# Optimization experiments

Measured on AMD Instinct MI355X. Metric: run time of the kernel, lower is better.

The kernel has to match this reference:

```python
import jax, jax.numpy as jnp
import numpy as np

N = 8192            # number of ROIs
FEAT = 255          # num_classes(151) + embed_dim(100) + pos_dim(4)
HID = 64
PRE_NMS = 6000      # eval-mode pre_nms_topn
POST_NMS = 300      # eval-mode post_nms_topn
NMS_THRESH = 0.7


def setup_inputs() -> dict:
    key = jax.random.key(0)
    ks = jax.random.split(key, 12)
    # rois: [N,5] = (im_ind, x1, y1, x2, y2), valid boxes in a 1024x1024 image
    x1 = jax.random.uniform(ks[0], (N,)) * 900.0
    y1 = jax.random.uniform(ks[1], (N,)) * 900.0
    w = jax.random.uniform(ks[2], (N,)) * 120.0 + 4.0
    h = jax.random.uniform(ks[3], (N,)) * 120.0 + 4.0
    rois = jnp.stack([jnp.zeros((N,)), x1, y1, x1 + w, y1 + h], axis=1).astype(jnp.float32)
    roi_feat = jax.random.normal(ks[4], (N, FEAT), dtype=jnp.float32)
    s = 0.05
    return {
        "rois": rois,
        "roi_feat": roi_feat,
        "W_sub1": jax.random.normal(ks[5], (FEAT, HID), jnp.float32) * s,
        "b_sub1": jnp.zeros((HID,), jnp.float32),
        "W_sub2": jax.random.normal(ks[6], (HID, HID), jnp.float32) * s,
        "b_sub2": jnp.zeros((HID,), jnp.float32),
        "W_obj1": jax.random.normal(ks[7], (FEAT, HID), jnp.float32) * s,
        "b_obj1": jnp.zeros((HID,), jnp.float32),
        "W_obj2": jax.random.normal(ks[8], (HID, HID), jnp.float32) * s,
        "b_obj2": jnp.zeros((HID,), jnp.float32),
    }


def _iou_matrix(boxes):
    # boxes: [K,4] (x1,y1,x2,y2) -> [K,K] IoU
    x1, y1, x2, y2 = boxes[:, 0], boxes[:, 1], boxes[:, 2], boxes[:, 3]
    area = (x2 - x1) * (y2 - y1)
    ix1 = jnp.maximum(x1[:, None], x1[None, :])
    iy1 = jnp.maximum(y1[:, None], y1[None, :])
    ix2 = jnp.minimum(x2[:, None], x2[None, :])
    iy2 = jnp.minimum(y2[:, None], y2[None, :])
    inter = jnp.maximum(ix2 - ix1, 0.0) * jnp.maximum(iy2 - iy1, 0.0)
    return inter / (area[:, None] + area[None, :] - inter + 1e-8)


def reference(rois, roi_feat, W_sub1, b_sub1, W_sub2, b_sub2,
              W_obj1, b_obj1, W_obj2, b_obj2):
    # Original detaches roi_feat before the bilinear head.
    f = jax.lax.stop_gradient(roi_feat)
    x_sub = jnp.maximum(f @ W_sub1 + b_sub1, 0.0) @ W_sub2 + b_sub2  # [N,64]
    x_obj = jnp.maximum(f @ W_obj1 + b_obj1, 0.0) @ W_obj2 + b_obj2  # [N,64]
    scores = jax.nn.sigmoid(x_sub @ x_obj.T)                          # [N,N]

    n = scores.shape[0]
    # exclude self-pairs (sub == obj)
    diag = jnp.arange(n)
    flat = scores.at[diag, diag].set(-1.0).reshape(-1)

    # pre-NMS top-k over all N*N pairs (sorted descending)
    top_s, top_i = jax.lax.top_k(flat, PRE_NMS)
    sub = top_i // n
    obj = top_i % n

    boxes = jax.lax.stop_gradient(rois[:, 1:5])
    bs, bo = boxes[sub], boxes[obj]
    # union box of each (sub,obj) pair for relation NMS
    union = jnp.concatenate([jnp.minimum(bs[:, :2], bo[:, :2]),
                             jnp.maximum(bs[:, 2:], bo[:, 2:])], axis=1)  # [PRE,4]
    iou = _iou_matrix(union)                                              # [PRE,PRE]
    # non-greedy (matrix) NMS: suppress i if any higher-ranked j overlaps > thresh
    higher = jnp.triu(jnp.ones((PRE_NMS, PRE_NMS), bool), k=1)  # [j,i] true when j < i
    suppressed = jnp.any((iou > NMS_THRESH) & higher, axis=0)
    kept_scores = jnp.where(suppressed, -1.0, top_s)

    post_s, post_k = jax.lax.top_k(kept_scores, POST_NMS)
    rel_inds = jnp.stack([sub[post_k], obj[post_k]], axis=1)  # [POST,2]
    return rel_inds, post_s
```

## Files before the change

kernel.cpp:

```cpp
#include <hip/hip_runtime.h>
#include <math.h>

#define NB    8192
#define FEAT  255
#define HID   64
#define TOPK  6000
#define POSTK 300
#define BINS  8192
#define BSHIFT 19
#define CAP   131072
#define CAPLIM 49152
#define SLACK 1
#define TSEL  1000
#define JSLICES 128
#define LCAP  2048
#define NMS_ICH 64

typedef __attribute__((ext_vector_type(8))) short bf16x8;
typedef __attribute__((ext_vector_type(4))) float f32x4;

__device__ __forceinline__ unsigned binOf(float x) {
    unsigned u = __float_as_uint(x);
    u = (u & 0x80000000u) ? ~u : (u | 0x80000000u);
    return u >> BSHIFT;
}

__device__ __forceinline__ unsigned short f2bf(float f) {
    unsigned u = __float_as_uint(f);
    return (unsigned short)((u + 0x7fffu + ((u >> 16) & 1u)) >> 16);
}

__global__ __launch_bounds__(256) void mlp_kernel(
    const float* __restrict__ feat,
    const float* __restrict__ W1s, const float* __restrict__ b1s,
    const float* __restrict__ W2s, const float* __restrict__ b2s,
    const float* __restrict__ W1o, const float* __restrict__ b1o,
    const float* __restrict__ W2o, const float* __restrict__ b2o,
    double* __restrict__ Xs64, double* __restrict__ Xo64,
    unsigned short* __restrict__ Xsb, unsigned short* __restrict__ Xob)
{
    int tid = threadIdx.x;
    int t   = tid & 63;
    int w   = tid >> 6;
    int rbase = blockIdx.x * 4;

    __shared__ double pS[4][4][64];
    __shared__ double pO[4][4][64];
    __shared__ double hs[4][64];
    __shared__ double ho[4][64];

    const float* f0 = feat + (size_t)(rbase + 0) * FEAT;
    const float* f1 = feat + (size_t)(rbase + 1) * FEAT;
    const float* f2 = feat + (size_t)(rbase + 2) * FEAT;
    const float* f3 = feat + (size_t)(rbase + 3) * FEAT;

    int kbeg = w * 64;
    int kend = kbeg + 64; if (kend > FEAT) kend = FEAT;
    double as[4] = {0, 0, 0, 0}, ao[4] = {0, 0, 0, 0};
#pragma unroll 4
    for (int k = kbeg; k < kend; ++k) {
        double ws = (double)W1s[k * HID + t];
        double wo = (double)W1o[k * HID + t];
        double g0 = (double)f0[k], g1 = (double)f1[k];
        double g2 = (double)f2[k], g3 = (double)f3[k];
        as[0] += g0 * ws; as[1] += g1 * ws; as[2] += g2 * ws; as[3] += g3 * ws;
        ao[0] += g0 * wo; ao[1] += g1 * wo; ao[2] += g2 * wo; ao[3] += g3 * wo;
    }
#pragma unroll
    for (int i = 0; i < 4; ++i) { pS[w][i][t] = as[i]; pO[w][i][t] = ao[i]; }
    __syncthreads();

    {
        double v = (double)b1s[t] + ((pS[0][w][t] + pS[1][w][t]) + (pS[2][w][t] + pS[3][w][t]));
        double u = (double)b1o[t] + ((pO[0][w][t] + pO[1][w][t]) + (pO[2][w][t] + pO[3][w][t]));
        hs[w][t] = v > 0.0 ? v : 0.0;
        ho[w][t] = u > 0.0 ? u : 0.0;
    }
    __syncthreads();

    int k2beg = w * 16, k2end = k2beg + 16;
    double xs[4] = {0, 0, 0, 0}, xo[4] = {0, 0, 0, 0};
#pragma unroll 4
    for (int k = k2beg; k < k2end; ++k) {
        double ws = (double)W2s[k * HID + t];
        double wo = (double)W2o[k * HID + t];
#pragma unroll
        for (int i = 0; i < 4; ++i) {
            xs[i] += hs[i][k] * ws;
            xo[i] += ho[i][k] * wo;
        }
    }
#pragma unroll
    for (int i = 0; i < 4; ++i) { pS[w][i][t] = xs[i]; pO[w][i][t] = xo[i]; }
    __syncthreads();

    {
        double v = (double)b2s[t] + ((pS[0][w][t] + pS[1][w][t]) + (pS[2][w][t] + pS[3][w][t]));
        double u = (double)b2o[t] + ((pO[0][w][t] + pO[1][w][t]) + (pO[2][w][t] + pO[3][w][t]));
        size_t o = (size_t)(rbase + w) * HID + t;
        Xs64[o] = v;
        Xo64[o] = u;
        Xsb[o] = f2bf((float)v);
        Xob[o] = f2bf((float)u);
    }
}

__global__ __launch_bounds__(256) void mfma_hist(
    const unsigned short* __restrict__ Xsb, const unsigned short* __restrict__ Xob,
    unsigned* __restrict__ ghist)
{
    __shared__ unsigned hist[BINS];
    int tid = threadIdx.x;
    for (int i = tid; i < BINS; i += 256) hist[i] = 0u;
    __syncthreads();

    int lane = tid & 63;
    int wave = tid >> 6;
    int quad = lane >> 4;
    int l16  = lane & 15;
    int r0 = blockIdx.y * 128 + (wave >> 1) * 64;
    int c0 = blockIdx.x * 128 + (wave & 1) * 64;

    f32x4 acc[4][4];
    bf16x8 afr[2][4], bfr[2][4];
#pragma unroll
    for (int kc = 0; kc < 2; ++kc)
#pragma unroll
        for (int t = 0; t < 4; ++t) {
            afr[kc][t] = *(const bf16x8*)(Xsb + (size_t)(r0 + t * 16 + l16) * HID + kc * 32 + quad * 8);
            bfr[kc][t] = *(const bf16x8*)(Xob + (size_t)(c0 + t * 16 + l16) * HID + kc * 32 + quad * 8);
        }
#pragma unroll
    for (int ti = 0; ti < 4; ++ti)
#pragma unroll
        for (int tj = 0; tj < 4; ++tj) acc[ti][tj] = (f32x4){0, 0, 0, 0};
#pragma unroll
    for (int kc = 0; kc < 2; ++kc)
#pragma unroll
        for (int ti = 0; ti < 4; ++ti)
#pragma unroll
            for (int tj = 0; tj < 4; ++tj)
                acc[ti][tj] = __builtin_amdgcn_mfma_f32_16x16x32_bf16(
                    afr[kc][ti], bfr[kc][tj], acc[ti][tj], 0, 0, 0);

#pragma unroll
    for (int ti = 0; ti < 4; ++ti)
#pragma unroll
        for (int tj = 0; tj < 4; ++tj)
#pragma unroll
            for (int i = 0; i < 4; ++i) {
                int r = r0 + ti * 16 + quad * 4 + i;
                int c = c0 + tj * 16 + l16;
                float v = acc[ti][tj][i];
                if (v > 0.0f && r != c)
                    atomicAdd(&hist[binOf(v)], 1u);
            }

    __syncthreads();
    for (int i = tid; i < BINS; i += 256) {
        unsigned h = hist[i];
        if (h) atomicAdd(&ghist[i], h);
    }
}

__global__ __launch_bounds__(256) void find_threshold(
    const unsigned* __restrict__ ghist, unsigned* __restrict__ ctrl)
{
    __shared__ unsigned csum[256];
    int tid  = threadIdx.x;
    int base = tid * (BINS / 256);
    unsigned s = 0;
    for (int i = 0; i < BINS / 256; ++i) s += ghist[base + i];
    csum[tid] = s;
    __syncthreads();
    if (tid == 0) {
        unsigned run = 0;
        for (int c = 255; c >= 0; --c) { run += csum[c]; csum[c] = run; }
    }
    __syncthreads();

    unsigned above = (tid == 255) ? 0u : csum[tid + 1];
    unsigned prev = above;
    for (int b = base + BINS / 256 - 1; b >= base; --b) {
        unsigned cur = prev + ghist[b];
        if (cur >= TSEL && prev < TSEL) {
            unsigned bstar = (unsigned)b;
            unsigned bt = bstar >= SLACK ? bstar - SLACK : 0;
            unsigned cnt = cur;
            for (unsigned bb = bstar; bb-- > bt;) cnt += ghist[bb];
            while (8u * cnt > CAPLIM && bt < bstar) { cnt -= ghist[bt]; bt++; }
            ctrl[1] = bt;
            unsigned key = bt << BSHIFT;
            unsigned fbits;
            if (key == 0u) fbits = 0xff800000u;
            else fbits = (key & 0x80000000u) ? (key ^ 0x80000000u) : ~key;
            ctrl[2] = fbits;
            break;
        }
        prev = cur;
    }
}

__global__ __launch_bounds__(256) void mfma_filter(
    const unsigned short* __restrict__ Xsb, const unsigned short* __restrict__ Xob,
    unsigned* __restrict__ ctrl, unsigned* __restrict__ cidx)
{
    __shared__ unsigned lcnt;
    __shared__ unsigned gbase;
    __shared__ unsigned lbuf[LCAP];
    float vt = __uint_as_float(ctrl[2]);
    int tid = threadIdx.x;
    if (tid == 0) lcnt = 0;

    int lane = tid & 63;
    int wave = tid >> 6;
    int quad = lane >> 4;
    int l16  = lane & 15;
    int r0 = blockIdx.y * 128 + (wave >> 1) * 64;
    int cb = blockIdx.x * 256 + (wave & 1) * 64;

    bf16x8 afr[2][4];
#pragma unroll
    for (int kc = 0; kc < 2; ++kc)
#pragma unroll
        for (int t = 0; t < 4; ++t)
            afr[kc][t] = *(const bf16x8*)(Xsb + (size_t)(r0 + t * 16 + l16) * HID + kc * 32 + quad * 8);

    bf16x8 bcur[2];
    {
        int col = cb + l16;
#pragma unroll
        for (int kc = 0; kc < 2; ++kc)
            bcur[kc] = *(const bf16x8*)(Xob + (size_t)col * HID + kc * 32 + quad * 8);
    }

    __syncthreads();

#pragma unroll
    for (int q = 0; q < 8; ++q) {
        int ct = q >> 2, tj = q & 3;
        int c0 = cb + ct * 128;
        int cj = c0 + tj * 16 + l16;
        bool nodiag = (r0 != c0);

        bf16x8 bnext[2];
        if (q < 7) {
            int q2 = q + 1;
            int col2 = cb + (q2 >> 2) * 128 + (q2 & 3) * 16 + l16;
#pragma unroll
            for (int kc = 0; kc < 2; ++kc)
                bnext[kc] = *(const bf16x8*)(Xob + (size_t)col2 * HID + kc * 32 + quad * 8);
        }

        f32x4 acc[4];
#pragma unroll
        for (int ti = 0; ti < 4; ++ti) acc[ti] = (f32x4){0, 0, 0, 0};
#pragma unroll
        for (int kc = 0; kc < 2; ++kc)
#pragma unroll
            for (int ti = 0; ti < 4; ++ti)
                acc[ti] = __builtin_amdgcn_mfma_f32_16x16x32_bf16(
                    afr[kc][ti], bcur[kc], acc[ti], 0, 0, 0);

        if (nodiag) {
#pragma unroll
            for (int ti = 0; ti < 4; ++ti)
#pragma unroll
                for (int i = 0; i < 4; ++i) {
                    if (acc[ti][i] >= vt) {
                        int r = r0 + ti * 16 + quad * 4 + i;
                        unsigned rc = (unsigned)r * (unsigned)NB + (unsigned)cj;
                        unsigned p = atomicAdd(&lcnt, 1u);
                        if (p < LCAP) {
                            lbuf[p] = rc;
                        } else {
                            unsigned g = atomicAdd(&ctrl[0], 1u);
                            if (g < CAP) cidx[g] = rc;
                        }
                    }
                }
        } else {
#pragma unroll
            for (int ti = 0; ti < 4; ++ti)
#pragma unroll
                for (int i = 0; i < 4; ++i) {
                    int r = r0 + ti * 16 + quad * 4 + i;
                    if (acc[ti][i] >= vt && r != cj) {
                        unsigned rc = (unsigned)r * (unsigned)NB + (unsigned)cj;
                        unsigned p = atomicAdd(&lcnt, 1u);
                        if (p < LCAP) {
                            lbuf[p] = rc;
                        } else {
                            unsigned g = atomicAdd(&ctrl[0], 1u);
                            if (g < CAP) cidx[g] = rc;
                        }
                    }
                }
        }

        if (q < 7) { bcur[0] = bnext[0]; bcur[1] = bnext[1]; }
    }

    __syncthreads();
    unsigned n = lcnt; if (n > LCAP) n = LCAP;
    if (tid == 0 && n) gbase = atomicAdd(&ctrl[0], n);
    __syncthreads();
    for (unsigned i = tid; i < n; i += 256u) {
        unsigned p = gbase + i;
        if (p < CAP) cidx[p] = lbuf[i];
    }
}

__global__ __launch_bounds__(256) void refine_kernel(
    const unsigned* __restrict__ ctrl, const unsigned* __restrict__ cidx,
    const double* __restrict__ Xs64, const double* __restrict__ Xo64,
    double* __restrict__ cval)
{
    unsigned M = ctrl[0];
    if (M > CAP) M = CAP;
    unsigned nw = gridDim.x * 4u;
    int lane = threadIdx.x & 63;
    for (unsigned w = blockIdx.x * 4u + (threadIdx.x >> 6); w < M; w += nw) {
        unsigned id = cidx[w];
        unsigned r = id >> 13, c = id & (NB - 1);
        double p = Xs64[(size_t)r * HID + lane] * Xo64[(size_t)c * HID + lane];
#pragma unroll
        for (int s = 32; s > 0; s >>= 1) p += __shfl_xor(p, s);
        if (lane == 0) cval[w] = (r == c) ? -1.0 : p;
    }
}

__global__ __launch_bounds__(256) void rank_count(
    const unsigned* __restrict__ ctrl,
    const double* __restrict__ cval, const unsigned* __restrict__ cidx,
    unsigned* __restrict__ rank)
{
    unsigned M = ctrl[0];
    if (M > CAP) M = CAP;

    unsigned slice = blockIdx.y;
    unsigned jbeg = (unsigned)(((unsigned long long)slice * M) / JSLICES);
    unsigned jend = (unsigned)(((unsigned long long)(slice + 1) * M) / JSLICES);

    __shared__ double  lv[256];
    __shared__ unsigned li[256];

    for (unsigned itile = blockIdx.x; itile * 1024u < M; itile += gridDim.x) {
        unsigned i0 = itile * 1024u + threadIdx.x;
        double v[4];
        unsigned id[4];
        unsigned cnt[4] = {0, 0, 0, 0};
#pragma unroll
        for (int k = 0; k < 4; ++k) {
            unsigned idx = i0 + (unsigned)k * 256u;
            bool a = idx < M;
            v[k]  = a ? cval[idx] : 0.0;
            id[k] = a ? cidx[idx] : 0u;
        }

        for (unsigned base = jbeg; base < jend; base += 256u) {
            unsigned j = base + threadIdx.x;
            if (j < jend) { lv[threadIdx.x] = cval[j]; li[threadIdx.x] = cidx[j]; }
            __syncthreads();
            unsigned lim = jend - base; if (lim > 256u) lim = 256u;
            for (unsigned e = 0; e < lim; ++e) {
                double ev = lv[e];
                unsigned ei = li[e];
#pragma unroll
                for (int k = 0; k < 4; ++k)
                    cnt[k] += (ev > v[k]) || (ev == v[k] && ei < id[k]);
            }
            __syncthreads();
        }
#pragma unroll
        for (int k = 0; k < 4; ++k) {
            unsigned idx = i0 + (unsigned)k * 256u;
            if (idx < M && cnt[k]) atomicAdd(&rank[idx], cnt[k]);
        }
    }
}

__global__ __launch_bounds__(256) void rank_scatter_prep(
    const unsigned* __restrict__ ctrl,
    const double* __restrict__ cval, const unsigned* __restrict__ cidx,
    const unsigned* __restrict__ rank, const float* __restrict__ rois,
    double* __restrict__ sval, unsigned* __restrict__ sidx,
    double* __restrict__ ub)
{
    unsigned M = ctrl[0];
    if (M > CAP) M = CAP;
    unsigned stride = gridDim.x * 256u;
    for (unsigned t = blockIdx.x * 256u + threadIdx.x; t < M; t += stride) {
        unsigned rk = rank[t];
        if (rk < TOPK) {
            unsigned id = cidx[t];
            sval[rk] = cval[t];
            sidx[rk] = id;
            unsigned s = id >> 13, o = id & (NB - 1);
            const float* bs = rois + (size_t)s * 5;
            const float* bo = rois + (size_t)o * 5;
            double x1 = fmin((double)bs[1], (double)bo[1]);
            double y1 = fmin((double)bs[2], (double)bo[2]);
            double x2 = fmax((double)bs[3], (double)bo[3]);
            double y2 = fmax((double)bs[4], (double)bo[4]);
            double area = (x2 - x1) * (y2 - y1);
            double* u = ub + (size_t)rk * 5;
            u[0] = x1; u[1] = y1; u[2] = x2; u[3] = y2; u[4] = 0.7 * area;
        }
    }
}

__global__ __launch_bounds__(256) void nms_kernel(
    const double* __restrict__ ub, unsigned* sup)
{
    int jb = blockIdx.x;
    int ic = blockIdx.y;
    int ibase = ic * NMS_ICH;
    if (ibase >= TOPK) return;
    if (ibase >= jb * 256 + 255) return;

    __shared__ double L[NMS_ICH][5];
    int tid = threadIdx.x;
    int icount = TOPK - ibase; if (icount > NMS_ICH) icount = NMS_ICH;
    for (int q = tid; q < icount * 5; q += 256)
        L[q / 5][q % 5] = ub[(size_t)ibase * 5 + q];
    __syncthreads();

    int j = jb * 256 + tid;
    if (j >= TOPK) return;
    int lim = j - ibase; if (lim > icount) lim = icount;
    if (lim <= 0) return;

    const double* u = ub + (size_t)j * 5;
    double x1 = u[0], y1 = u[1], x2 = u[2], y2 = u[3], pa = u[4];
    bool flag = false;
    for (int e = 0; e < lim; ++e) {
        double ix1 = fmax(L[e][0], x1);
        double iy1 = fmax(L[e][1], y1);
        double ix2 = fmin(L[e][2], x2);
        double iy2 = fmin(L[e][3], y2);
        double iw = ix2 - ix1; iw = iw > 0.0 ? iw : 0.0;
        double ih = iy2 - iy1; ih = ih > 0.0 ? ih : 0.0;
        flag |= (1.7 * (iw * ih) > pa + L[e][4] + 7e-9);
    }
    if (flag) sup[j] = 1u;
}

__global__ __launch_bounds__(1024) void finalize_kernel(
    const unsigned* __restrict__ sup, const double* __restrict__ sval,
    const unsigned* __restrict__ sidx, float* __restrict__ out)
{
    __shared__ unsigned wsum[16];
    __shared__ unsigned red[16];
    __shared__ unsigned bases[2];
    __shared__ unsigned totalu_s;
    int tid  = threadIdx.x;
    int lane = tid & 63;
    int w    = tid >> 6;

    unsigned s = 0;
    for (int i = tid; i < TOPK; i += 1024) s += (sup[i] == 0u);
#pragma unroll
    for (int st = 32; st > 0; st >>= 1) s += __shfl_down(s, st);
    if (lane == 0) red[w] = s;
    __syncthreads();
    if (tid == 0) {
        unsigned tot = 0;
        for (int i = 0; i < 16; ++i) tot += red[i];
        totalu_s = tot; bases[0] = 0; bases[1] = 0;
    }
    __syncthreads();
    unsigned totalu = totalu_s;

    for (int c = 0; c < (TOPK + 1023) / 1024; ++c) {
        int idx = c * 1024 + tid;
        int valid = TOPK - c * 1024; if (valid > 1024) valid = 1024;
        unsigned f = (idx < TOPK && sup[idx] == 0u) ? 1u : 0u;
        unsigned long long m = __ballot(f != 0u);
        if (lane == 0) wsum[w] = (unsigned)__popcll(m);
        __syncthreads();
        unsigned wbase = 0, ctot = 0;
        for (int i = 0; i < 16; ++i) {
            unsigned v = wsum[i];
            if (i < w) wbase += v;
            ctot += v;
        }
        unsigned e = wbase + (unsigned)__popcll(m & ((1ull << lane) - 1ull));
        if (idx < TOPK) {
            unsigned pos = f ? (bases[0] + e)
                             : (totalu + bases[1] + (unsigned)tid - e);
            if (pos < POSTK) {
                unsigned id = sidx[idx];
                unsigned sb = id >> 13, ob = id & (NB - 1);
                out[2 * pos]     = (float)sb;
                out[2 * pos + 1] = (float)ob;
                double sg = f ? 1.0 / (1.0 + exp(-sval[idx])) : -1.0;
                out[2 * POSTK + pos] = (float)sg;
            }
        }
        __syncthreads();
        if (tid == 0) {
            bases[0] += ctot;
            bases[1] += (unsigned)valid - ctot;
        }
        __syncthreads();
    }
}

extern "C" void kernel_launch(void* const* d_in, const int* in_sizes, int n_in,
                              void* d_out, int out_size, void* d_ws, size_t ws_size,
                              hipStream_t stream)
{
    const float* rois = (const float*)d_in[0];
    const float* feat = (const float*)d_in[1];
    const float* W1s  = (const float*)d_in[2];
    const float* b1s  = (const float*)d_in[3];
    const float* W2s  = (const float*)d_in[4];
    const float* b2s  = (const float*)d_in[5];
    const float* W1o  = (const float*)d_in[6];
    const float* b1o  = (const float*)d_in[7];
    const float* W2o  = (const float*)d_in[8];
    const float* b2o  = (const float*)d_in[9];

    char* ws = (char*)d_ws;
    size_t off = 0;
    auto alloc = [&](size_t bytes) -> void* {
        off = (off + 255) & ~(size_t)255;
        void* p = ws + off;
        off += bytes;
        return p;
    };

    unsigned* ghist = (unsigned*)alloc((size_t)BINS * 4);
    unsigned* ctrl  = (unsigned*)alloc(256);
    unsigned* sup   = (unsigned*)alloc((size_t)6144 * 4);
    unsigned* rank  = (unsigned*)alloc((size_t)CAP * 4);
    size_t zero_bytes = off;

    double* Xs64 = (double*)alloc((size_t)NB * HID * 8);
    double* Xo64 = (double*)alloc((size_t)NB * HID * 8);
    unsigned short* Xsb = (unsigned short*)alloc((size_t)NB * HID * 2);
    unsigned short* Xob = (unsigned short*)alloc((size_t)NB * HID * 2);
    double* cval = (double*)alloc((size_t)CAP * 8);
    unsigned* cidx = (unsigned*)alloc((size_t)CAP * 4);
    double* svalv = (double*)alloc((size_t)TOPK * 8);
    unsigned* sidxv = (unsigned*)alloc((size_t)TOPK * 4);
    double* ub   = (double*)alloc((size_t)TOPK * 5 * 8);

    hipMemsetAsync(d_ws, 0, zero_bytes, stream);

    mlp_kernel<<<NB / 4, 256, 0, stream>>>(feat, W1s, b1s, W2s, b2s,
                                           W1o, b1o, W2o, b2o,
                                           Xs64, Xo64, Xsb, Xob);
    mfma_hist<<<dim3(8, 64), 256, 0, stream>>>(Xsb, Xob, ghist);
    find_threshold<<<1, 256, 0, stream>>>(ghist, ctrl);
    mfma_filter<<<dim3(32, 64), 256, 0, stream>>>(Xsb, Xob, ctrl, cidx);
    refine_kernel<<<2048, 256, 0, stream>>>(ctrl, cidx, Xs64, Xo64, cval);
    rank_count<<<dim3(16, JSLICES), 256, 0, stream>>>(ctrl, cval, cidx, rank);
    rank_scatter_prep<<<512, 256, 0, stream>>>(ctrl, cval, cidx, rank, rois,
                                               svalv, sidxv, ub);
    nms_kernel<<<dim3((TOPK + 255) / 256, (TOPK + NMS_ICH - 1) / NMS_ICH), 256, 0, stream>>>(ub, sup);
    finalize_kernel<<<1, 1024, 0, stream>>>(sup, svalv, sidxv, (float*)d_out);
}
```

Baseline: 246.7 us.

## Compute MLP layers with FP64 MFMA on 16-row tiles staged in LDS

Rewrites the two-layer MLP kernel so each block handles 16 ROIs. The feature rows are staged in shared memory, and both linear layers run on the 16x16x4 FP64 MFMA instruction. Each wave computes one network (sub or obj) for a 32-column slice instead of doing scalar FP64 FMAs. This is meant to cut the FP64 ALU cost and the redundant weight loads of the old 4-row scalar version. The trade-off is a different summation order, which can change double-precision results slightly, and fewer blocks in the grid.

```diff
diff --git a/kernel.cpp b/kernel.cpp
--- a/kernel.cpp
+++ b/kernel.cpp
@@ -18,6 +18,7 @@
 
 typedef __attribute__((ext_vector_type(8))) short bf16x8;
 typedef __attribute__((ext_vector_type(4))) float f32x4;
+typedef __attribute__((ext_vector_type(4))) double f64x4;
 
 __device__ __forceinline__ unsigned binOf(float x) {
     unsigned u = __float_as_uint(x);
@@ -39,69 +40,96 @@
     double* __restrict__ Xs64, double* __restrict__ Xo64,
     unsigned short* __restrict__ Xsb, unsigned short* __restrict__ Xob)
 {
-    int tid = threadIdx.x;
-    int t   = tid & 63;
-    int w   = tid >> 6;
-    int rbase = blockIdx.x * 4;
-
-    __shared__ double pS[4][4][64];
-    __shared__ double pO[4][4][64];
-    __shared__ double hs[4][64];
-    __shared__ double ho[4][64];
-
-    const float* f0 = feat + (size_t)(rbase + 0) * FEAT;
-    const float* f1 = feat + (size_t)(rbase + 1) * FEAT;
-    const float* f2 = feat + (size_t)(rbase + 2) * FEAT;
-    const float* f3 = feat + (size_t)(rbase + 3) * FEAT;
-
-    int kbeg = w * 64;
-    int kend = kbeg + 64; if (kend > FEAT) kend = FEAT;
-    double as[4] = {0, 0, 0, 0}, ao[4] = {0, 0, 0, 0};
+    __shared__ float  fl[16 * 258];
+    __shared__ double hl[2][16][65];
+
+    int tid  = threadIdx.x;
+    int lane = tid & 63;
+    int w    = tid >> 6;
+    int a16  = lane & 15;
+    int kq   = lane >> 4;
+    int net  = w & 1;
+    int p    = w >> 1;
+    int rbase = blockIdx.x * 16;
+
+    const float* fsrc = feat + (size_t)rbase * FEAT;
+    for (int idx = tid; idx < 16 * FEAT; idx += 256) {
+        int r = idx / FEAT;
+        int k = idx - r * FEAT;
+        fl[r * 258 + k] = fsrc[idx];
+    }
+    if (tid < 16) fl[tid * 258 + 255] = 0.0f;
+    __syncthreads();
+
+    const float* W1 = net ? W1o : W1s;
+    const float* B1 = net ? b1o : b1s;
+    const float* W2 = net ? W2o : W2s;
+    const float* B2 = net ? b2o : b2s;
+    double*       X  = net ? Xo64 : Xs64;
+    unsigned short* Xb = net ? Xob : Xsb;
+
+    int c0 = (2 * p) * 16 + a16;
+    int c1 = (2 * p + 1) * 16 + a16;
+
+    f64x4 acc0 = {0, 0, 0, 0}, acc1 = {0, 0, 0, 0};
 #pragma unroll 4
-    for (int k = kbeg; k < kend; ++k) {
-        double ws = (double)W1s[k * HID + t];
-        double wo = (double)W1o[k * HID + t];
-        double g0 = (double)f0[k], g1 = (double)f1[k];
-        double g2 = (double)f2[k], g3 = (double)f3[k];
-        as[0] += g0 * ws; as[1] += g1 * ws; as[2] += g2 * ws; as[3] += g3 * ws;
-        ao[0] += g0 * wo; ao[1] += g1 * wo; ao[2] += g2 * wo; ao[3] += g3 * wo;
-    }
-#pragma unroll
-    for (int i = 0; i < 4; ++i) { pS[w][i][t] = as[i]; pO[w][i][t] = ao[i]; }
-    __syncthreads();
-
+    for (int ks = 0; ks < 63; ++ks) {
+        int k = ks * 4 + kq;
+        double av = (double)fl[a16 * 258 + k];
+        double b0 = (double)W1[k * HID + c0];
+        double b1 = (double)W1[k * HID + c1];
+        acc0 = __builtin_amdgcn_mfma_f64_16x16x4f64(av, b0, acc0, 0, 0, 0);
+        acc1 = __builtin_amdgcn_mfma_f64_16x16x4f64(av, b1, acc1, 0, 0, 0);
+    }
     {
-        double v = (double)b1s[t] + ((pS[0][w][t] + pS[1][w][t]) + (pS[2][w][t] + pS[3][w][t]));
-        double u = (double)b1o[t] + ((pO[0][w][t] + pO[1][w][t]) + (pO[2][w][t] + pO[3][w][t]));
-        hs[w][t] = v > 0.0 ? v : 0.0;
-        ho[w][t] = u > 0.0 ? u : 0.0;
-    }
-    __syncthreads();
-
-    int k2beg = w * 16, k2end = k2beg + 16;
-    double xs[4] = {0, 0, 0, 0}, xo[4] = {0, 0, 0, 0};
+        int k = 252 + kq;
+        double av = (double)fl[a16 * 258 + k];
+        double b0 = 0.0, b1 = 0.0;
+        if (k < FEAT) {
+            b0 = (double)W1[k * HID + c0];
+            b1 = (double)W1[k * HID + c1];
+        }
+        acc0 = __builtin_amdgcn_mfma_f64_16x16x4f64(av, b0, acc0, 0, 0, 0);
+        acc1 = __builtin_amdgcn_mfma_f64_16x16x4f64(av, b1, acc1, 0, 0, 0);
+    }
+
+    {
+        double bb0 = (double)B1[c0], bb1 = (double)B1[c1];
+#pragma unroll
+        for (int i = 0; i < 4; ++i) {
+            int r = kq * 4 + i;
+            double v0 = acc0[i] + bb0;
+            double v1 = acc1[i] + bb1;
+            hl[net][r][c0] = v0 > 0.0 ? v0 : 0.0;
+            hl[net][r][c1] = v1 > 0.0 ? v1 : 0.0;
+        }
+    }
+    __syncthreads();
+
+    f64x4 x0 = {0, 0, 0, 0}, x1 = {0, 0, 0, 0};
 #pragma unroll 4
-    for (int k = k2beg; k < k2end; ++k) {
-        double ws = (double)W2s[k * HID + t];
-        double wo = (double)W2o[k * HID + t];
+    for (int ks = 0; ks < 16; ++ks) {
+        int k = ks * 4 + kq;
+        double av = hl[net][a16][k];
+        double b0 = (double)W2[k * HID + c0];
+        double b1 = (double)W2[k * HID + c1];
+        x0 = __builtin_amdgcn_mfma_f64_16x16x4f64(av, b0, x0, 0, 0, 0);
+        x1 = __builtin_amdgcn_mfma_f64_16x16x4f64(av, b1, x1, 0, 0, 0);
+    }
+
+    {
+        double bb0 = (double)B2[c0], bb1 = (double)B2[c1];
 #pragma unroll
         for (int i = 0; i < 4; ++i) {
-            xs[i] += hs[i][k] * ws;
-            xo[i] += ho[i][k] * wo;
-        }
-    }
-#pragma unroll
-    for (int i = 0; i < 4; ++i) { pS[w][i][t] = xs[i]; pO[w][i][t] = xo[i]; }
-    __syncthreads();
-
-    {
-        double v = (double)b2s[t] + ((pS[0][w][t] + pS[1][w][t]) + (pS[2][w][t] + pS[3][w][t]));
-        double u = (double)b2o[t] + ((pO[0][w][t] + pO[1][w][t]) + (pO[2][w][t] + pO[3][w][t]));
-        size_t o = (size_t)(rbase + w) * HID + t;
-        Xs64[o] = v;
-        Xo64[o] = u;
-        Xsb[o] = f2bf((float)v);
-        Xob[o] = f2bf((float)u);
+            int r = kq * 4 + i;
+            double v0 = x0[i] + bb0;
+            double v1 = x1[i] + bb1;
+            size_t o0 = (size_t)(rbase + r) * HID + c0;
+            size_t o1 = (size_t)(rbase + r) * HID + c1;
+            X[o0] = v0; X[o1] = v1;
+            Xb[o0] = f2bf((float)v0);
+            Xb[o1] = f2bf((float)v1);
+        }
     }
 }
 
@@ -549,9 +577,9 @@
 
     hipMemsetAsync(d_ws, 0, zero_bytes, stream);
 
-    mlp_kernel<<<NB / 4, 256, 0, stream>>>(feat, W1s, b1s, W2s, b2s,
-                                           W1o, b1o, W2o, b2o,
-                                           Xs64, Xo64, Xsb, Xob);
+    mlp_kernel<<<NB / 16, 256, 0, stream>>>(feat, W1s, b1s, W2s, b2s,
+                                            W1o, b1o, W2o, b2o,
+                                            Xs64, Xo64, Xsb, Xob);
     mfma_hist<<<dim3(8, 64), 256, 0, stream>>>(Xsb, Xob, ghist);
     find_threshold<<<1, 256, 0, stream>>>(ghist, ctrl);
     mfma_filter<<<dim3(32, 64), 256, 0, stream>>>(Xsb, Xob, ctrl, cidx);
```

Measured after the change: 230.0 us. 6.8% less time.
